# Kernel optimization log

Measured on AMD Instinct MI355X. Metric: run time of the kernel, lower is better.

The kernel has to match this reference:

```python
import jax, jax.numpy as jnp
import numpy as np

# ctlib options layout: [views, dets, width, height, dImg, dDet, Ang0, dAng, s2r, d2r, binshift]
VIEWS = 512
DETS = 512
H_IMG = 256
W_IMG = 256
D_IMG = 0.006641
D_DET = 0.0072
ANG0 = 0.0
D_ANG = 2.0 * np.pi / VIEWS
S2R = 5.95
D2R = 4.906
VIRDET = D_DET * S2R / (S2R + D2R)  # virtual detector spacing at isocenter


def make_filter():
    # ramp (Ram-Lak) filter in spatial domain, length 2*dets-1
    x = np.arange(2 * DETS - 1) - DETS + 1
    x2 = np.where(x == 0, 1, x * x).astype(np.float64)
    f = np.where(np.abs(x) % 2 == 1, -1.0 / (np.pi ** 2 * x2 * VIRDET ** 2), 0.0)
    f = np.where(x == 0, 1.0 / (4.0 * VIRDET ** 2), f)
    return jnp.asarray(f, dtype=jnp.float32).reshape(1, 1, 1, -1)


def make_w():
    # cosine (distance) pre-weight * quadrature step (virdet * pi / views)
    u = (np.arange(DETS) - DETS / 2 + 0.5) * VIRDET
    w = S2R / np.sqrt(S2R ** 2 + u ** 2) * VIRDET * np.pi / VIEWS
    return jnp.asarray(w, dtype=jnp.float32).reshape(1, 1, 1, -1)


def setup_inputs() -> dict:
    key = jax.random.key(0)
    projection = jax.random.normal(key, (2, 1, VIEWS, DETS), dtype=jnp.float32)
    return {"projection": projection, "w": make_w(), "filt": make_filter()}


def ramp_filter(p, filt):
    # p: [B,1,V,D], filt: [1,1,1,2D-1] -> [B,1,V,D] (same padding along detector axis)
    return jax.lax.conv_general_dilated(
        p, filt, window_strides=(1, 1),
        padding=((0, 0), (DETS - 1, DETS - 1)),
        dimension_numbers=("NCHW", "OIHW", "NCHW"))


def backproject_sv(p):
    # pixel-driven equidistant fan-beam backprojection, one output channel per view
    # p: [B,1,V,D] -> [B,V,H,W]
    p3 = p[:, 0]  # [B,V,D]
    betas = ANG0 + D_ANG * jnp.arange(VIEWS, dtype=jnp.float32)
    cb = jnp.cos(betas)[:, None, None]  # [V,1,1]
    sb = jnp.sin(betas)[:, None, None]
    xs = ((jnp.arange(W_IMG, dtype=jnp.float32) - (W_IMG - 1) / 2.0) * D_IMG)[None, None, :]
    ys = (((H_IMG - 1) / 2.0 - jnp.arange(H_IMG, dtype=jnp.float32)) * D_IMG)[None, :, None]
    d = S2R - (xs * cb + ys * sb)               # [V,H,W] source-to-pixel depth
    u = S2R * (ys * cb - xs * sb) / d           # virtual-detector coordinate
    wgt = (S2R / d) ** 2                        # fan-beam U^{-2} weight
    t = u / VIRDET + (DETS - 1) / 2.0           # fractional detector index
    i0 = jnp.floor(t).astype(jnp.int32)
    frac = t - i0
    v0 = (i0 >= 0) & (i0 < DETS)
    v1 = (i0 + 1 >= 0) & (i0 + 1 < DETS)
    i0c = jnp.clip(i0, 0, DETS - 1)
    i1c = jnp.clip(i0 + 1, 0, DETS - 1)
    gather = jax.vmap(lambda pv, idx: pv[:, idx], in_axes=(1, 0), out_axes=1)
    vals0 = gather(p3, i0c)  # [B,V,H,W]
    vals1 = gather(p3, i1c)
    w0 = ((1.0 - frac) * v0)[None]
    w1 = (frac * v1)[None]
    return wgt[None] * (vals0 * w0 + vals1 * w1)


def reference(projection, w, filt):
    p = projection * w                 # per-detector ramp pre-weight
    p = ramp_filter(p, filt)           # full-width ramp convolution
    return backproject_sv(p)           # per-view backprojection [B,V,H,W]
```

## Files before the change

kernel.cpp:

```cpp
#include <hip/hip_runtime.h>
#include <math.h>

#define VIEWS 512
#define DETS  512

typedef float f32x4 __attribute__((ext_vector_type(4)));

constexpr double S2R_D    = 5.95;
constexpr double D2R_D    = 4.906;
constexpr double DDET_D   = 0.0072;
constexpr double VIRDET_D = DDET_D * S2R_D / (S2R_D + D2R_D);
constexpr double DANG_D   = 2.0 * 3.14159265358979323846 / (double)VIEWS;

__global__ __launch_bounds__(256) void fbp_filter_kernel(
    const float* __restrict__ proj, const float* __restrict__ wq,
    const float* __restrict__ filt, float* __restrict__ wsf,
    float* __restrict__ trig)
{
    __shared__ __align__(16) float pwpad[2][1536];
    __shared__ __align__(16) float sfe[520];
    const int tid = threadIdx.x;
    const int bid = blockIdx.x;

    if (bid < 2) {
        int v = bid * 256 + tid;
        float beta = (float)DANG_D * (float)v;
        trig[v]         = cosf(beta);
        trig[VIEWS + v] = sinf(beta);
    }

    for (int i = tid; i < 520; i += 256)
        sfe[i] = (i < 512) ? filt[2 * i] : 0.0f;

    float4* pz = (float4*)&pwpad[0][0];
    #pragma unroll
    for (int i = 0; i < 3; ++i)
        pz[tid + 256 * i] = make_float4(0.f, 0.f, 0.f, 0.f);
    __syncthreads();

    {
        const int rl  = tid >> 7;
        const int t2  = tid & 127;
        const int row = bid * 2 + rl;
        const float4 p4 = *(const float4*)(proj + (size_t)row * DETS + 4 * t2);
        const float4 w4 = *(const float4*)(wq + 4 * t2);
        pwpad[rl][511 + 4 * t2 + 0] = p4.x * w4.x;
        pwpad[rl][511 + 4 * t2 + 1] = p4.y * w4.y;
        pwpad[rl][511 + 4 * t2 + 2] = p4.z * w4.z;
        pwpad[rl][511 + 4 * t2 + 3] = p4.w * w4.w;
    }
    __syncthreads();

    const int lane = tid & 63;
    const int warp = tid >> 6;
    const int rl2  = warp >> 1;
    const int wv   = warp & 1;
    const int d0   = 256 * wv + 4 * lane;
    const float* P = &pwpad[rl2][0];
    const int e_lo = wv ? 0 : 124;
    const int G    = wv ? 48 : 49;
    const float c0 = filt[511];

    float a0 = 0.f, a1 = 0.f, a2 = 0.f, a3 = 0.f;
    for (int g = 0; g < G; ++g) {
        const int e0 = e_lo + 8 * g;
        const float4 S0 = *(const float4*)&sfe[e0];
        const float4 S1 = *(const float4*)&sfe[e0 + 4];
        const float* Pb = P + d0 + 2 * e0;
        const float4 q0 = *(const float4*)(Pb + 0);
        const float4 q1 = *(const float4*)(Pb + 4);
        const float4 q2 = *(const float4*)(Pb + 8);
        const float4 q3 = *(const float4*)(Pb + 12);
        const float4 q4 = *(const float4*)(Pb + 16);
        const float p[20] = {q0.x,q0.y,q0.z,q0.w, q1.x,q1.y,q1.z,q1.w,
                             q2.x,q2.y,q2.z,q2.w, q3.x,q3.y,q3.z,q3.w,
                             q4.x,q4.y,q4.z,q4.w};
        const float s[8]  = {S0.x,S0.y,S0.z,S0.w, S1.x,S1.y,S1.z,S1.w};
        #pragma unroll
        for (int j = 0; j < 8; ++j) {
            a0 = fmaf(p[2*j + 0], s[j], a0);
            a1 = fmaf(p[2*j + 1], s[j], a1);
            a2 = fmaf(p[2*j + 2], s[j], a2);
            a3 = fmaf(p[2*j + 3], s[j], a3);
        }
    }
    a0 = fmaf(P[511 + d0 + 0], c0, a0);
    a1 = fmaf(P[511 + d0 + 1], c0, a1);
    a2 = fmaf(P[511 + d0 + 2], c0, a2);
    a3 = fmaf(P[511 + d0 + 3], c0, a3);

    const int row2 = bid * 2 + rl2;
    *(float4*)(wsf + (size_t)row2 * DETS + d0) = make_float4(a0, a1, a2, a3);
}

__global__ __launch_bounds__(256) void fbp_bp_kernel(
    const float* __restrict__ wsf, const float* __restrict__ trig,
    float* __restrict__ out)
{
    __shared__ __align__(16) float rows[2][DETS];
    const int tid = threadIdx.x;
    const int v  = blockIdx.x >> 3;
    const int yc = blockIdx.x & 7;

    {
        const float* src = wsf + (((size_t)(tid >> 7) * VIEWS + v) << 9);
        ((float4*)&rows[0][0])[tid] = ((const float4*)src)[tid & 127];
    }
    const float cb = trig[v];
    const float sb = trig[VIEWS + v];
    __syncthreads();

    const int xi = (tid & 63) * 4;
    const int wv = tid >> 6;
    const float xs0 = ((float)xi - 127.5f) * 0.006641f;
    const float xc0 = xs0 * cb;
    const float xs_sb0 = xs0 * sb;
    const float dcb = 0.006641f * cb;
    const float dsb = 0.006641f * sb;

    #pragma unroll
    for (int i = 0; i < 8; ++i) {
        const int y = yc * 32 + i * 4 + wv;
        const float ys = (127.5f - (float)y) * 0.006641f;
        const float ysb = ys * sb;
        const float ycb = ys * cb;
        f32x4 o0, o1;
        #pragma unroll
        for (int j = 0; j < 4; ++j) {
            const float xcb = xc0 + (float)j * dcb;
            const float xsb = xs_sb0 + (float)j * dsb;
            const float den = 5.95f - xcb - ysb;
            float inv = __builtin_amdgcn_rcpf(den);
            inv = inv * (2.0f - den * inv);
            const float sw  = 5.95f * inv;
            const float wgt = sw * sw;
            const float u   = 5.95f * (ycb - xsb) * inv;
            const float t   = u * (float)(1.0 / VIRDET_D) + 255.5f;
            const float ft  = floorf(t);
            const int   i0  = (int)ft;
            const float fr  = t - ft;
            const float w0 = (i0 >= 0 && i0 < DETS)         ? (1.0f - fr) : 0.0f;
            const float w1 = (i0 + 1 >= 0 && i0 + 1 < DETS) ? fr          : 0.0f;
            const int i0c = min(max(i0, 0), DETS - 1);
            const int i1c = min(max(i0 + 1, 0), DETS - 1);
            o0[j] = wgt * (rows[0][i0c] * w0 + rows[0][i1c] * w1);
            o1[j] = wgt * (rows[1][i0c] * w0 + rows[1][i1c] * w1);
        }
        const size_t pix = (((size_t)v << 16) + ((size_t)y << 8) + (size_t)xi) >> 2;
        __builtin_nontemporal_store(o0, (f32x4*)out + pix);
        __builtin_nontemporal_store(o1, (f32x4*)out + 8388608u + pix);
    }
}

extern "C" void kernel_launch(void* const* d_in, const int* in_sizes, int n_in,
                              void* d_out, int out_size, void* d_ws, size_t ws_size,
                              hipStream_t stream) {
    const float* proj = (const float*)d_in[0];
    const float* wq   = (const float*)d_in[1];
    const float* filt = (const float*)d_in[2];
    float* out  = (float*)d_out;
    float* wsf  = (float*)d_ws;
    float* trig = wsf + (size_t)1024 * 512;

    hipLaunchKernelGGL(fbp_filter_kernel, dim3(512), dim3(256), 0, stream,
                       proj, wq, filt, wsf, trig);
    hipLaunchKernelGGL(fbp_bp_kernel, dim3(VIEWS * 8), dim3(256), 0, stream,
                       wsf, trig, out);
}
```

Baseline: 288.8 us.

## Fuse ramp filter and backprojection into one per-view kernel

Merges the filter and backprojection kernels into one launch with a block per view. Each block filters both batch rows for its view in shared memory, then backprojects all 256 image rows from that buffer. This removes the workspace round trip, the trig table and the second launch. The filtered rows are stored interleaved and zero-padded so each bilinear tap is one 2-float load with no bounds checks. The trade-off is 512 blocks instead of 4096, with each block doing far more serial work, which may reduce latency hiding for the store-bound output.

```diff
diff --git a/kernel.cpp b/kernel.cpp
--- a/kernel.cpp
+++ b/kernel.cpp
@@ -5,150 +5,141 @@
 #define DETS  512
 
 typedef float f32x4 __attribute__((ext_vector_type(4)));
+typedef float f32x2 __attribute__((ext_vector_type(2)));
 
 constexpr double S2R_D    = 5.95;
 constexpr double D2R_D    = 4.906;
 constexpr double DDET_D   = 0.0072;
 constexpr double VIRDET_D = DDET_D * S2R_D / (S2R_D + D2R_D);
 constexpr double DANG_D   = 2.0 * 3.14159265358979323846 / (double)VIEWS;
+constexpr double DIMG_D   = 0.006641;
 
-__global__ __launch_bounds__(256) void fbp_filter_kernel(
+__global__ __launch_bounds__(256) void fbp_fused_kernel(
     const float* __restrict__ proj, const float* __restrict__ wq,
-    const float* __restrict__ filt, float* __restrict__ wsf,
-    float* __restrict__ trig)
+    const float* __restrict__ filt, float* __restrict__ out)
 {
     __shared__ __align__(16) float pwpad[2][1536];
     __shared__ __align__(16) float sfe[520];
+    __shared__ __align__(16) float rows01[1536];
+
     const int tid = threadIdx.x;
-    const int bid = blockIdx.x;
+    const int v   = blockIdx.x;
 
-    if (bid < 2) {
-        int v = bid * 256 + tid;
-        float beta = (float)DANG_D * (float)v;
-        trig[v]         = cosf(beta);
-        trig[VIEWS + v] = sinf(beta);
+    const float beta = (float)DANG_D * (float)v;
+    const float cb = cosf(beta);
+    const float sb = sinf(beta);
+
+    {
+        const f32x4 z = {0.f, 0.f, 0.f, 0.f};
+        f32x4* pz = (f32x4*)&pwpad[0][0];
+        #pragma unroll
+        for (int i = 0; i < 3; ++i) pz[tid + 256*i] = z;
+        f32x4* rz = (f32x4*)rows01;
+        rz[tid] = z;
+        if (tid < 128) rz[256 + tid] = z;
+        for (int i = tid; i < 520; i += 256)
+            sfe[i] = (i < 512) ? filt[2*i] : 0.0f;
     }
-
-    for (int i = tid; i < 520; i += 256)
-        sfe[i] = (i < 512) ? filt[2 * i] : 0.0f;
-
-    float4* pz = (float4*)&pwpad[0][0];
-    #pragma unroll
-    for (int i = 0; i < 3; ++i)
-        pz[tid + 256 * i] = make_float4(0.f, 0.f, 0.f, 0.f);
     __syncthreads();
 
     {
         const int rl  = tid >> 7;
         const int t2  = tid & 127;
-        const int row = bid * 2 + rl;
-        const float4 p4 = *(const float4*)(proj + (size_t)row * DETS + 4 * t2);
-        const float4 w4 = *(const float4*)(wq + 4 * t2);
-        pwpad[rl][511 + 4 * t2 + 0] = p4.x * w4.x;
-        pwpad[rl][511 + 4 * t2 + 1] = p4.y * w4.y;
-        pwpad[rl][511 + 4 * t2 + 2] = p4.z * w4.z;
-        pwpad[rl][511 + 4 * t2 + 3] = p4.w * w4.w;
+        const int row = rl * VIEWS + v;
+        const f32x4 p4 = *(const f32x4*)(proj + ((size_t)row << 9) + 4*t2);
+        const f32x4 w4 = *(const f32x4*)(wq + 4*t2);
+        pwpad[rl][511 + 4*t2 + 0] = p4.x * w4.x;
+        pwpad[rl][511 + 4*t2 + 1] = p4.y * w4.y;
+        pwpad[rl][511 + 4*t2 + 2] = p4.z * w4.z;
+        pwpad[rl][511 + 4*t2 + 3] = p4.w * w4.w;
     }
     __syncthreads();
 
     const int lane = tid & 63;
     const int warp = tid >> 6;
-    const int rl2  = warp >> 1;
-    const int wv   = warp & 1;
-    const int d0   = 256 * wv + 4 * lane;
-    const float* P = &pwpad[rl2][0];
-    const int e_lo = wv ? 0 : 124;
-    const int G    = wv ? 48 : 49;
-    const float c0 = filt[511];
-
-    float a0 = 0.f, a1 = 0.f, a2 = 0.f, a3 = 0.f;
-    for (int g = 0; g < G; ++g) {
-        const int e0 = e_lo + 8 * g;
-        const float4 S0 = *(const float4*)&sfe[e0];
-        const float4 S1 = *(const float4*)&sfe[e0 + 4];
-        const float* Pb = P + d0 + 2 * e0;
-        const float4 q0 = *(const float4*)(Pb + 0);
-        const float4 q1 = *(const float4*)(Pb + 4);
-        const float4 q2 = *(const float4*)(Pb + 8);
-        const float4 q3 = *(const float4*)(Pb + 12);
-        const float4 q4 = *(const float4*)(Pb + 16);
-        const float p[20] = {q0.x,q0.y,q0.z,q0.w, q1.x,q1.y,q1.z,q1.w,
-                             q2.x,q2.y,q2.z,q2.w, q3.x,q3.y,q3.z,q3.w,
-                             q4.x,q4.y,q4.z,q4.w};
-        const float s[8]  = {S0.x,S0.y,S0.z,S0.w, S1.x,S1.y,S1.z,S1.w};
-        #pragma unroll
-        for (int j = 0; j < 8; ++j) {
-            a0 = fmaf(p[2*j + 0], s[j], a0);
-            a1 = fmaf(p[2*j + 1], s[j], a1);
-            a2 = fmaf(p[2*j + 2], s[j], a2);
-            a3 = fmaf(p[2*j + 3], s[j], a3);
-        }
-    }
-    a0 = fmaf(P[511 + d0 + 0], c0, a0);
-    a1 = fmaf(P[511 + d0 + 1], c0, a1);
-    a2 = fmaf(P[511 + d0 + 2], c0, a2);
-    a3 = fmaf(P[511 + d0 + 3], c0, a3);
-
-    const int row2 = bid * 2 + rl2;
-    *(float4*)(wsf + (size_t)row2 * DETS + d0) = make_float4(a0, a1, a2, a3);
-}
-
-__global__ __launch_bounds__(256) void fbp_bp_kernel(
-    const float* __restrict__ wsf, const float* __restrict__ trig,
-    float* __restrict__ out)
-{
-    __shared__ __align__(16) float rows[2][DETS];
-    const int tid = threadIdx.x;
-    const int v  = blockIdx.x >> 3;
-    const int yc = blockIdx.x & 7;
 
     {
-        const float* src = wsf + (((size_t)(tid >> 7) * VIEWS + v) << 9);
-        ((float4*)&rows[0][0])[tid] = ((const float4*)src)[tid & 127];
+        const int rl2 = warp >> 1;
+        const int wv  = warp & 1;
+        const int d0  = 256*wv + 4*lane;
+        const float* P = &pwpad[rl2][0];
+        const int e_lo = wv ? 0 : 124;
+        const int G    = wv ? 48 : 49;
+        const float c0 = filt[511];
+        float a0=0.f, a1=0.f, a2=0.f, a3=0.f;
+        for (int g = 0; g < G; ++g) {
+            const int e0 = e_lo + 8*g;
+            const f32x4 S0 = *(const f32x4*)&sfe[e0];
+            const f32x4 S1 = *(const f32x4*)&sfe[e0 + 4];
+            const float* Pb = P + d0 + 2*e0;
+            const f32x4 q0 = *(const f32x4*)(Pb + 0);
+            const f32x4 q1 = *(const f32x4*)(Pb + 4);
+            const f32x4 q2 = *(const f32x4*)(Pb + 8);
+            const f32x4 q3 = *(const f32x4*)(Pb + 12);
+            const f32x4 q4 = *(const f32x4*)(Pb + 16);
+            const float p[20] = {q0.x,q0.y,q0.z,q0.w, q1.x,q1.y,q1.z,q1.w,
+                                 q2.x,q2.y,q2.z,q2.w, q3.x,q3.y,q3.z,q3.w,
+                                 q4.x,q4.y,q4.z,q4.w};
+            const float s[8]  = {S0.x,S0.y,S0.z,S0.w, S1.x,S1.y,S1.z,S1.w};
+            #pragma unroll
+            for (int j = 0; j < 8; ++j) {
+                a0 = fmaf(p[2*j + 0], s[j], a0);
+                a1 = fmaf(p[2*j + 1], s[j], a1);
+                a2 = fmaf(p[2*j + 2], s[j], a2);
+                a3 = fmaf(p[2*j + 3], s[j], a3);
+            }
+        }
+        a0 = fmaf(P[511 + d0 + 0], c0, a0);
+        a1 = fmaf(P[511 + d0 + 1], c0, a1);
+        a2 = fmaf(P[511 + d0 + 2], c0, a2);
+        a3 = fmaf(P[511 + d0 + 3], c0, a3);
+        float* W = &rows01[((128 + d0) << 1) + rl2];
+        W[0] = a0; W[2] = a1; W[4] = a2; W[6] = a3;
     }
-    const float cb = trig[v];
-    const float sb = trig[VIEWS + v];
     __syncthreads();
 
-    const int xi = (tid & 63) * 4;
-    const int wv = tid >> 6;
-    const float xs0 = ((float)xi - 127.5f) * 0.006641f;
-    const float xc0 = xs0 * cb;
-    const float xs_sb0 = xs0 * sb;
-    const float dcb = 0.006641f * cb;
-    const float dsb = 0.006641f * sb;
+    {
+        const float D    = (float)DIMG_D;
+        const float Kf   = (float)(S2R_D / VIRDET_D);
+        const int   xi   = 4*lane;
+        const float xs0  = ((float)xi - 127.5f) * D;
+        const float xc0  = xs0 * cb;
+        const float xsbK = (xs0 * sb) * Kf;
+        const float dcb  = D * cb;
+        const float dsbK = (D * sb) * Kf;
+        const f32x2* R2  = (const f32x2*)rows01;
+        f32x4* o0p = (f32x4*)(out + ((size_t)v << 16));
 
-    #pragma unroll
-    for (int i = 0; i < 8; ++i) {
-        const int y = yc * 32 + i * 4 + wv;
-        const float ys = (127.5f - (float)y) * 0.006641f;
-        const float ysb = ys * sb;
-        const float ycb = ys * cb;
-        f32x4 o0, o1;
-        #pragma unroll
-        for (int j = 0; j < 4; ++j) {
-            const float xcb = xc0 + (float)j * dcb;
-            const float xsb = xs_sb0 + (float)j * dsb;
-            const float den = 5.95f - xcb - ysb;
-            float inv = __builtin_amdgcn_rcpf(den);
-            inv = inv * (2.0f - den * inv);
-            const float sw  = 5.95f * inv;
-            const float wgt = sw * sw;
-            const float u   = 5.95f * (ycb - xsb) * inv;
-            const float t   = u * (float)(1.0 / VIRDET_D) + 255.5f;
-            const float ft  = floorf(t);
-            const int   i0  = (int)ft;
-            const float fr  = t - ft;
-            const float w0 = (i0 >= 0 && i0 < DETS)         ? (1.0f - fr) : 0.0f;
-            const float w1 = (i0 + 1 >= 0 && i0 + 1 < DETS) ? fr          : 0.0f;
-            const int i0c = min(max(i0, 0), DETS - 1);
-            const int i1c = min(max(i0 + 1, 0), DETS - 1);
-            o0[j] = wgt * (rows[0][i0c] * w0 + rows[0][i1c] * w1);
-            o1[j] = wgt * (rows[1][i0c] * w0 + rows[1][i1c] * w1);
+        #pragma unroll 2
+        for (int i = 0; i < 64; ++i) {
+            const int   y   = 4*i + warp;
+            const float ys  = (127.5f - (float)y) * D;
+            const float ysb = ys * sb;
+            const float ycb = ys * cb;
+            const float dbase = (5.95f - ysb) - xc0;
+            const float nbase = fmaf(Kf, ycb, -xsbK);
+            f32x4 o0, o1;
+            #pragma unroll
+            for (int j = 0; j < 4; ++j) {
+                const float jf  = (float)j;
+                const float den = fmaf(jf, -dcb,  dbase);
+                const float num = fmaf(jf, -dsbK, nbase);
+                float inv = __builtin_amdgcn_rcpf(den);
+                inv = inv * fmaf(-den, inv, 2.0f);
+                const float wgt = 35.4025f * (inv * inv);
+                const float t   = fmaf(num, inv, 383.5f);
+                const float ft  = floorf(t);
+                const float fr  = t - ft;
+                const int   idx = (int)ft;
+                const f32x2 ab  = R2[idx];
+                const f32x2 cd  = R2[idx + 1];
+                o0[j] = wgt * fmaf(fr, cd.x - ab.x, ab.x);
+                o1[j] = wgt * fmaf(fr, cd.y - ab.y, ab.y);
+            }
+            const size_t p4i = ((size_t)y << 6) + (size_t)lane;
+            __builtin_nontemporal_store(o0, o0p + p4i);
+            __builtin_nontemporal_store(o1, o0p + 8388608u + p4i);
         }
-        const size_t pix = (((size_t)v << 16) + ((size_t)y << 8) + (size_t)xi) >> 2;
-        __builtin_nontemporal_store(o0, (f32x4*)out + pix);
-        __builtin_nontemporal_store(o1, (f32x4*)out + 8388608u + pix);
     }
 }
 
@@ -158,12 +149,9 @@
     const float* proj = (const float*)d_in[0];
     const float* wq   = (const float*)d_in[1];
     const float* filt = (const float*)d_in[2];
-    float* out  = (float*)d_out;
-    float* wsf  = (float*)d_ws;
-    float* trig = wsf + (size_t)1024 * 512;
+    float* out = (float*)d_out;
+    (void)in_sizes; (void)n_in; (void)out_size; (void)d_ws; (void)ws_size;
 
-    hipLaunchKernelGGL(fbp_filter_kernel, dim3(512), dim3(256), 0, stream,
-                       proj, wq, filt, wsf, trig);
-    hipLaunchKernelGGL(fbp_bp_kernel, dim3(VIEWS * 8), dim3(256), 0, stream,
-                       wsf, trig, out);
+    hipLaunchKernelGGL(fbp_fused_kernel, dim3(VIEWS), dim3(256), 0, stream,
+                       proj, wq, filt, out);
 }
```

Measured after the change: 278.5 us. 1.04x faster.
